# Optimization experiments

Measured on AMD Instinct MI355X. Metric: run time of the kernel, lower is better.

The kernel has to match this reference:

```python
import jax, jax.numpy as jnp
import numpy as np

S = 9                 # graphlet_size
N = 2 * S + 1         # 19 wires -> 2^19 statevector
DEPTH = 1             # entangling_depth
C64 = jnp.complex64

_INV_SQRT2 = 1.0 / np.sqrt(2.0)
H_GATE = jnp.array([[_INV_SQRT2, _INV_SQRT2], [_INV_SQRT2, -_INV_SQRT2]], dtype=C64)
CNOT = jnp.array([[1, 0, 0, 0], [0, 1, 0, 0], [0, 0, 0, 1], [0, 0, 1, 0]], dtype=C64)


def _rx(t):
    c = jnp.cos(t / 2).astype(C64)
    s = (-1j * jnp.sin(t / 2)).astype(C64)
    return jnp.stack([jnp.stack([c, s]), jnp.stack([s, c])])


def _ry(t):
    c = jnp.cos(t / 2).astype(C64)
    s = jnp.sin(t / 2).astype(C64)
    return jnp.stack([jnp.stack([c, -s]), jnp.stack([s, c])])


def _rz(t):
    em = jnp.exp(-0.5j * t).astype(C64)
    ep = jnp.exp(0.5j * t).astype(C64)
    z = jnp.zeros((), C64)
    return jnp.stack([jnp.stack([em, z]), jnp.stack([z, ep])])


def _ctrl(U):
    # 4x4 controlled gate: identity on control=0 block, U on control=1 block
    M = jnp.zeros((4, 4), C64).at[0, 0].set(1.0).at[1, 1].set(1.0)
    return M.at[2:, 2:].set(U)


def apply_1q(psi, U, w):
    psi = jnp.moveaxis(psi, w, 0)
    psi = jnp.tensordot(U, psi, axes=1)
    return jnp.moveaxis(psi, 0, w)


def apply_2q(psi, U, w0, w1):
    # w0 = control (first wire), w1 = target, torchquantum wire order
    psi = jnp.moveaxis(psi, (w0, w1), (0, 1))
    shp = psi.shape
    psi = (U @ psi.reshape(4, -1)).reshape(shp)
    return jnp.moveaxis(psi, (0, 1), (w0, w1))


def strong_block(psi, params, wires):
    depth, nq = params.shape[0], len(wires)
    for d in range(depth):
        for qi, w in enumerate(wires):
            psi = apply_1q(psi, _rz(params[d, qi, 0]), w)
            psi = apply_1q(psi, _ry(params[d, qi, 1]), w)
            psi = apply_1q(psi, _rx(params[d, qi, 2]), w)
        for i in range(nq - 1):
            psi = apply_2q(psi, CNOT, wires[i], wires[i + 1])
        if nq >= 3:
            psi = apply_2q(psi, CNOT, wires[-1], wires[0])
    return psi


def _circuit(inputs_flat, inits, strong0_params, strong1_params, update_params):
    feat = inputs_flat.reshape(-1, 2)
    num_edges = S - 1
    adj = feat[:num_edges]            # [S-1, 2]
    vert = feat[num_edges:num_edges + S]  # [S, 2]

    psi = jnp.zeros((2,) * N, C64).at[(0,) * N].set(1.0)

    # encode_features
    for i in range(num_edges):
        psi = apply_1q(psi, _ry(adj[i, 0]), i)
        psi = apply_1q(psi, _rz(adj[i, 1]), i)
    center = S - 1
    for i in range(S):
        psi = apply_1q(psi, _ry(vert[i, 0]), center + i)
        psi = apply_1q(psi, _rz(vert[i, 1]), center + i)

    anc1, anc2 = 2 * S - 1, 2 * S
    # message blocks per edge
    for i in range(num_edges):
        edge = i
        neighbor = center + i + 1
        psi = apply_2q(psi, _ctrl(_rx(inits[0, 0])), neighbor, anc1)
        psi = apply_2q(psi, _ctrl(_ry(inits[0, 1])), edge, anc1)
        psi = apply_2q(psi, _ctrl(_rz(inits[0, 2])), neighbor, anc2)
        psi = apply_2q(psi, _ctrl(_ry(inits[0, 3])), edge, anc2)
        psi = strong_block(psi, strong0_params, [edge, neighbor, anc1])
        psi = strong_block(psi, strong1_params, [anc1, neighbor, anc2])

    # update block
    psi = strong_block(psi, update_params, [center, anc1, anc2])

    # expval_x_scalar: Hadamard on center, then Z-like sign sum.
    # Original flattens the torchquantum state (wire 0 = MSB) and reads bit
    # `center` from the LSB, which is tensor axis N-1-center.
    psi = apply_1q(psi, H_GATE, center)
    axis = N - 1 - center
    sign = (1.0 - 2.0 * jnp.arange(2, dtype=jnp.float32)).reshape(
        (1,) * axis + (2,) + (1,) * (N - 1 - axis))
    probs = psi.real ** 2 + psi.imag ** 2
    return jnp.sum(probs * sign).reshape(1)


def setup_inputs() -> dict:
    key = jax.random.key(0)
    k1, k2, k3, k4, k5 = jax.random.split(key, 5)
    pi = float(np.pi)
    return {
        "inputs_flat": jax.random.uniform(k1, ((2 * S - 1) * 2,), jnp.float32),
        "inits": jax.random.uniform(k2, (1, 4), jnp.float32, 0.0, pi),
        "strong0_params": jax.random.uniform(k3, (DEPTH, 3, 3), jnp.float32, 0.0, pi),
        "strong1_params": jax.random.uniform(k4, (DEPTH, 3, 3), jnp.float32, 0.0, pi),
        "update_params": jax.random.uniform(k5, (DEPTH, 3, 3), jnp.float32, 0.0, pi),
    }


def reference(inputs_flat, inits, strong0_params, strong1_params, update_params):
    return _circuit(inputs_flat, inits, strong0_params, strong1_params, update_params)
```

## Files before the change

kernel.cpp:

```cpp
#include <hip/hip_runtime.h>
#include <math.h>


struct cplx { float x, y; };
__device__ __forceinline__ cplx cmul(cplx a, cplx b){ return {a.x*b.x - a.y*b.y, a.x*b.y + a.y*b.x}; }
__device__ __forceinline__ cplx cadd(cplx a, cplx b){ return {a.x+b.x, a.y+b.y}; }

__device__ __forceinline__ void mat2mul(const cplx* A, const cplx* B, cplx* C){
  C[0] = cadd(cmul(A[0],B[0]), cmul(A[1],B[2]));
  C[1] = cadd(cmul(A[0],B[1]), cmul(A[1],B[3]));
  C[2] = cadd(cmul(A[2],B[0]), cmul(A[3],B[2]));
  C[3] = cadd(cmul(A[2],B[1]), cmul(A[3],B[3]));
}
__device__ void mk_rz(float t, cplx* M){ float s,c; sincosf(0.5f*t,&s,&c); M[0]={c,-s};M[1]={0,0};M[2]={0,0};M[3]={c,s}; }
__device__ void mk_ry(float t, cplx* M){ float s,c; sincosf(0.5f*t,&s,&c); M[0]={c,0};M[1]={-s,0};M[2]={s,0};M[3]={c,0}; }
__device__ void mk_rx(float t, cplx* M){ float s,c; sincosf(0.5f*t,&s,&c); M[0]={c,0};M[1]={0,-s};M[2]={0,-s};M[3]={c,0}; }
__device__ void mk_strong(const float* p, cplx* M){
  cplx Rz[4],Ry[4],Rx[4],T[4];
  mk_rz(p[0],Rz); mk_ry(p[1],Ry); mk_rx(p[2],Rx);
  mat2mul(Ry,Rz,T); mat2mul(Rx,T,M);
}

__device__ __forceinline__ cplx spin(float ty, float tz, int bit){
  float sy,cy,sz,cz;
  sincosf(0.5f*ty,&sy,&cy);
  sincosf(0.5f*tz,&sz,&cz);
  return bit ? cplx{sy*cz, sy*sz} : cplx{cy*cz, -cy*sz};
}

__device__ __forceinline__ cplx shxor(cplx a, int m){
  return { __shfl_xor(a.x, m), __shfl_xor(a.y, m) };
}

__device__ __forceinline__ void rot(cplx& amp, int lane, int b, const cplx* M, int c = -1){
  cplx p = shxor(amp, 1 << b);
  bool hi = (lane >> b) & 1;
  cplx lo_ = hi ? p : amp;
  cplx hi_ = hi ? amp : p;
  cplx na = hi ? cadd(cmul(M[2], lo_), cmul(M[3], hi_))
               : cadd(cmul(M[0], lo_), cmul(M[1], hi_));
  if (c >= 0 && !((lane >> c) & 1)) na = amp;
  amp = na;
}
__device__ __forceinline__ void cnot(cplx& amp, int lane, int c, int t){
  cplx p = shxor(amp, 1 << t);
  if ((lane >> c) & 1) amp = p;
}

__global__ __launch_bounds__(64)
void qlightcone(const float* __restrict__ inf, const float* __restrict__ inits,
                const float* __restrict__ s0p, const float* __restrict__ s1p,
                float* __restrict__ out)
{
  const int lane = threadIdx.x;

  cplx Mcrx[4],Mcry1[4],Mcrz[4],Mcry2[4];
  mk_rx(inits[0],Mcrx); mk_ry(inits[1],Mcry1); mk_rz(inits[2],Mcrz); mk_ry(inits[3],Mcry2);
  cplx S0e[4],S0n[4],S0a[4],S1a[4],S1n[4],S1x[4];
  mk_strong(s0p+0,S0e); mk_strong(s0p+3,S0n); mk_strong(s0p+6,S0a);
  mk_strong(s1p+0,S1a); mk_strong(s1p+3,S1n); mk_strong(s1p+6,S1x);

  cplx amp = {0.f, 0.f};
  if ((lane & 3) == 0){
    cplx a = cmul(spin(inf[0],  inf[1],  (lane >> 5) & 1),
                  spin(inf[2],  inf[3],  (lane >> 4) & 1));
    cplx b = cmul(spin(inf[18], inf[19], (lane >> 3) & 1),
                  spin(inf[20], inf[21], (lane >> 2) & 1));
    amp = cmul(a, b);
  }

  #pragma unroll
  for (int p = 0; p < 2; ++p){
    const int eb = 5 - p, nb = 3 - p;
    rot(amp, lane, 1, Mcrx,  nb);
    rot(amp, lane, 1, Mcry1, eb);
    rot(amp, lane, 0, Mcrz,  nb);
    rot(amp, lane, 0, Mcry2, eb);
    rot(amp, lane, eb, S0e);
    rot(amp, lane, nb, S0n);
    rot(amp, lane, 1,  S0a);
    cnot(amp, lane, eb, nb);
    cnot(amp, lane, nb, 1);
    cnot(amp, lane, 1,  eb);
    rot(amp, lane, 1,  S1a);
    rot(amp, lane, nb, S1n);
    rot(amp, lane, 0,  S1x);
    cnot(amp, lane, 1,  nb);
    cnot(amp, lane, nb, 0);
    cnot(amp, lane, 0,  1);
  }

  float s = amp.x*amp.x + amp.y*amp.y;
  if ((lane >> 2) & 1) s = -s;
  for (int off = 32; off > 0; off >>= 1) s += __shfl_down(s, off);
  if (lane == 0) out[0] = s;
}

extern "C" void kernel_launch(void* const* d_in, const int* in_sizes, int n_in,
                              void* d_out, int out_size, void* d_ws, size_t ws_size,
                              hipStream_t stream) {
  const float* inf   = (const float*)d_in[0];
  const float* inits = (const float*)d_in[1];
  const float* s0p   = (const float*)d_in[2];
  const float* s1p   = (const float*)d_in[3];
  float* out = (float*)d_out;

  qlightcone<<<dim3(1), dim3(64), 0, stream>>>(inf, inits, s0p, s1p, out);
}
```

Measured before the change: 65.63 us.

## Build gate matrices in parallel across lanes and drive gates from an opcode table

Each of the ten 2x2 gate matrices is now built by its own lane using a shared generic Rz·Ry·Rx formula, then stored in LDS. Before, every thread computed all ten matrices serially. The unrolled gate sequence becomes a rolled loop over a 32-entry opcode table in device memory, which shrinks code size at the cost of runtime decode, table loads and LDS reads. Fast __sinf/__cosf intrinsics replace sincosf, which may reduce accuracy slightly.

```diff
diff --git a/kernel.cpp b/kernel.cpp
--- a/kernel.cpp
+++ b/kernel.cpp
@@ -5,46 +5,28 @@
 struct cplx { float x, y; };
 __device__ __forceinline__ cplx cmul(cplx a, cplx b){ return {a.x*b.x - a.y*b.y, a.x*b.y + a.y*b.x}; }
 __device__ __forceinline__ cplx cadd(cplx a, cplx b){ return {a.x+b.x, a.y+b.y}; }
-
 __device__ __forceinline__ void mat2mul(const cplx* A, const cplx* B, cplx* C){
   C[0] = cadd(cmul(A[0],B[0]), cmul(A[1],B[2]));
   C[1] = cadd(cmul(A[0],B[1]), cmul(A[1],B[3]));
   C[2] = cadd(cmul(A[2],B[0]), cmul(A[3],B[2]));
   C[3] = cadd(cmul(A[2],B[1]), cmul(A[3],B[3]));
 }
-__device__ void mk_rz(float t, cplx* M){ float s,c; sincosf(0.5f*t,&s,&c); M[0]={c,-s};M[1]={0,0};M[2]={0,0};M[3]={c,s}; }
-__device__ void mk_ry(float t, cplx* M){ float s,c; sincosf(0.5f*t,&s,&c); M[0]={c,0};M[1]={-s,0};M[2]={s,0};M[3]={c,0}; }
-__device__ void mk_rx(float t, cplx* M){ float s,c; sincosf(0.5f*t,&s,&c); M[0]={c,0};M[1]={0,-s};M[2]={0,-s};M[3]={c,0}; }
-__device__ void mk_strong(const float* p, cplx* M){
-  cplx Rz[4],Ry[4],Rx[4],T[4];
-  mk_rz(p[0],Rz); mk_ry(p[1],Ry); mk_rx(p[2],Rx);
-  mat2mul(Ry,Rz,T); mat2mul(Rx,T,M);
-}
+
+#define OPR(b,m,c) (unsigned short)(((m)<<9)|((c)<<5)|((b)<<1))
+#define OPC(c,t)   (unsigned short)(((c)<<5)|((t)<<1)|1)
+#define PASS(eb,nb) \
+  OPR(1,0,nb), OPR(1,1,eb), OPR(0,2,nb), OPR(0,3,eb), \
+  OPR(eb,4,15), OPR(nb,5,15), OPR(1,6,15), \
+  OPC(eb,nb), OPC(nb,1), OPC(1,eb), \
+  OPR(1,7,15), OPR(nb,8,15), OPR(0,9,15), \
+  OPC(1,nb), OPC(nb,0), OPC(0,1)
+
+__device__ const unsigned short OPS[32] = { PASS(5,3), PASS(4,2) };
 
 __device__ __forceinline__ cplx spin(float ty, float tz, int bit){
-  float sy,cy,sz,cz;
-  sincosf(0.5f*ty,&sy,&cy);
-  sincosf(0.5f*tz,&sz,&cz);
+  float sy = __sinf(0.5f*ty), cy = __cosf(0.5f*ty);
+  float sz = __sinf(0.5f*tz), cz = __cosf(0.5f*tz);
   return bit ? cplx{sy*cz, sy*sz} : cplx{cy*cz, -cy*sz};
-}
-
-__device__ __forceinline__ cplx shxor(cplx a, int m){
-  return { __shfl_xor(a.x, m), __shfl_xor(a.y, m) };
-}
-
-__device__ __forceinline__ void rot(cplx& amp, int lane, int b, const cplx* M, int c = -1){
-  cplx p = shxor(amp, 1 << b);
-  bool hi = (lane >> b) & 1;
-  cplx lo_ = hi ? p : amp;
-  cplx hi_ = hi ? amp : p;
-  cplx na = hi ? cadd(cmul(M[2], lo_), cmul(M[3], hi_))
-               : cadd(cmul(M[0], lo_), cmul(M[1], hi_));
-  if (c >= 0 && !((lane >> c) & 1)) na = amp;
-  amp = na;
-}
-__device__ __forceinline__ void cnot(cplx& amp, int lane, int c, int t){
-  cplx p = shxor(amp, 1 << t);
-  if ((lane >> c) & 1) amp = p;
 }
 
 __global__ __launch_bounds__(64)
@@ -52,46 +34,65 @@
                 const float* __restrict__ s0p, const float* __restrict__ s1p,
                 float* __restrict__ out)
 {
+  __shared__ float2 Mlds[10][4];
   const int lane = threadIdx.x;
 
-  cplx Mcrx[4],Mcry1[4],Mcrz[4],Mcry2[4];
-  mk_rx(inits[0],Mcrx); mk_ry(inits[1],Mcry1); mk_rz(inits[2],Mcrz); mk_ry(inits[3],Mcry2);
-  cplx S0e[4],S0n[4],S0a[4],S1a[4],S1n[4],S1x[4];
-  mk_strong(s0p+0,S0e); mk_strong(s0p+3,S0n); mk_strong(s0p+6,S0a);
-  mk_strong(s1p+0,S1a); mk_strong(s1p+3,S1n); mk_strong(s1p+6,S1x);
-
-  cplx amp = {0.f, 0.f};
-  if ((lane & 3) == 0){
-    cplx a = cmul(spin(inf[0],  inf[1],  (lane >> 5) & 1),
-                  spin(inf[2],  inf[3],  (lane >> 4) & 1));
-    cplx b = cmul(spin(inf[18], inf[19], (lane >> 3) & 1),
-                  spin(inf[20], inf[21], (lane >> 2) & 1));
-    amp = cmul(a, b);
+  {
+    const int ml = (lane < 10) ? lane : 4;
+    float tx = 0.f, ty = 0.f, tz = 0.f;
+    if (ml < 4){
+      float a = inits[ml];
+      tx = (ml == 0) ? a : 0.f;
+      ty = (ml == 1 || ml == 3) ? a : 0.f;
+      tz = (ml == 2) ? a : 0.f;
+    } else {
+      const float* pp = (ml < 7) ? s0p + 3*(ml - 4) : s1p + 3*(ml - 7);
+      tz = pp[0]; ty = pp[1]; tx = pp[2];
+    }
+    float sx = __sinf(0.5f*tx), cx = __cosf(0.5f*tx);
+    float sy = __sinf(0.5f*ty), cy = __cosf(0.5f*ty);
+    float sz = __sinf(0.5f*tz), cz = __cosf(0.5f*tz);
+    cplx Rz[4] = {{cz,-sz},{0,0},{0,0},{cz,sz}};
+    cplx Ry[4] = {{cy,0},{-sy,0},{sy,0},{cy,0}};
+    cplx Rx[4] = {{cx,0},{0,-sx},{0,-sx},{cx,0}};
+    cplx T[4], M[4];
+    mat2mul(Ry, Rz, T); mat2mul(Rx, T, M);
+    if (lane < 10){
+      #pragma unroll
+      for (int j = 0; j < 4; ++j) Mlds[lane][j] = make_float2(M[j].x, M[j].y);
+    }
   }
 
-  #pragma unroll
-  for (int p = 0; p < 2; ++p){
-    const int eb = 5 - p, nb = 3 - p;
-    rot(amp, lane, 1, Mcrx,  nb);
-    rot(amp, lane, 1, Mcry1, eb);
-    rot(amp, lane, 0, Mcrz,  nb);
-    rot(amp, lane, 0, Mcry2, eb);
-    rot(amp, lane, eb, S0e);
-    rot(amp, lane, nb, S0n);
-    rot(amp, lane, 1,  S0a);
-    cnot(amp, lane, eb, nb);
-    cnot(amp, lane, nb, 1);
-    cnot(amp, lane, 1,  eb);
-    rot(amp, lane, 1,  S1a);
-    rot(amp, lane, nb, S1n);
-    rot(amp, lane, 0,  S1x);
-    cnot(amp, lane, 1,  nb);
-    cnot(amp, lane, nb, 0);
-    cnot(amp, lane, 0,  1);
+  cplx amp = cmul(cmul(spin(inf[0],  inf[1],  (lane >> 5) & 1),
+                       spin(inf[2],  inf[3],  (lane >> 4) & 1)),
+                  cmul(spin(inf[18], inf[19], (lane >> 3) & 1),
+                       spin(inf[20], inf[21], (lane >> 2) & 1)));
+  if (lane & 3) amp = {0.f, 0.f};
+  __syncthreads();
+
+  for (int i = 0; i < 32; ++i){
+    const int op   = OPS[i];
+    const int b    = (op >> 1) & 15;
+    const int c    = (op >> 5) & 15;
+    const cplx p   = { __shfl_xor(amp.x, 1 << b), __shfl_xor(amp.y, 1 << b) };
+    const bool cok = (c == 15) || ((lane >> c) & 1);
+    if (op & 1){
+      if (cok) amp = p;
+    } else {
+      const int m = (op >> 9) & 15;
+      float2 f0 = Mlds[m][0], f1 = Mlds[m][1], f2 = Mlds[m][2], f3 = Mlds[m][3];
+      const bool hi = (lane >> b) & 1;
+      cplx lo_ = hi ? p : amp, hi_ = hi ? amp : p;
+      cplx A = hi ? cplx{f2.x,f2.y} : cplx{f0.x,f0.y};
+      cplx B = hi ? cplx{f3.x,f3.y} : cplx{f1.x,f1.y};
+      cplx na = cadd(cmul(A, lo_), cmul(B, hi_));
+      if (cok) amp = na;
+    }
   }
 
   float s = amp.x*amp.x + amp.y*amp.y;
   if ((lane >> 2) & 1) s = -s;
+  #pragma unroll
   for (int off = 32; off > 0; off >>= 1) s += __shfl_down(s, off);
   if (lane == 0) out[0] = s;
 }
```

New measurement: 62.63 us. 4.6% less time.
